# Optimization experiments

Measured on AMD Instinct MI355X. Metric: run time of the kernel, lower is better.

Reference implementation:

```python
import jax, jax.numpy as jnp
import numpy as np

IN_CH = 128
N_HEAD = 16
D_K = 4
D_MODEL = 256
T_PE = 1000.0
EPS = 1e-5


def setup_inputs() -> dict:
    key = jax.random.key(0)
    ks = jax.random.split(key, 8)
    sz_b, L, h, w = 4, 30, 64, 64
    x = jax.random.normal(ks[0], (sz_b, L, IN_CH, h, w), dtype=jnp.float32)
    batch_positions = jnp.sort(jax.random.randint(ks[1], (sz_b, L), 0, 365), axis=1).astype(jnp.int32)
    pad_mask = jnp.zeros((sz_b, L), dtype=bool)
    gn_weight = jnp.ones((IN_CH,), dtype=jnp.float32)
    gn_bias = jnp.zeros((IN_CH,), dtype=jnp.float32)
    conv_w = jax.random.normal(ks[2], (D_MODEL, IN_CH), dtype=jnp.float32) * (1.0 / np.sqrt(IN_CH))
    conv_b = jnp.zeros((D_MODEL,), dtype=jnp.float32)
    Q = jax.random.normal(ks[3], (N_HEAD, D_K), dtype=jnp.float32) * np.sqrt(2.0 / D_K)
    Wk = jax.random.normal(ks[4], (N_HEAD * D_K, D_MODEL), dtype=jnp.float32) * np.sqrt(2.0 / D_K)
    bk = jnp.zeros((N_HEAD * D_K,), dtype=jnp.float32)
    return {"x": x, "gn_weight": gn_weight, "gn_bias": gn_bias,
            "conv_w": conv_w, "conv_b": conv_b, "Q": Q, "Wk": Wk, "bk": bk,
            "batch_positions": batch_positions, "pad_mask": pad_mask}


def reference(x, gn_weight, gn_bias, conv_w, conv_b, Q, Wk, bk, batch_positions, pad_mask):
    n_head, d_k = Q.shape
    sz_b, L, d, h, w = x.shape
    B = sz_b * h * w
    # flatten pixels: [B, L, C]
    out = x.transpose(0, 3, 4, 1, 2).reshape(B, L, d)
    # GroupNorm(num_groups=n_head) over channels and time per pixel-sample
    g = out.transpose(0, 2, 1).reshape(B, n_head, d // n_head, L)
    mu = g.mean(axis=(2, 3), keepdims=True)
    var = g.var(axis=(2, 3), keepdims=True)
    g = (g - mu) / jnp.sqrt(var + EPS)
    out = g.reshape(B, d, L) * gn_weight[None, :, None] + gn_bias[None, :, None]
    out = out.transpose(0, 2, 1)  # [B, L, C]
    # 1x1 Conv1d == per-timestep linear projection to d_model
    out = out @ conv_w.T + conv_b  # [B, L, d_model]
    d_model = conv_w.shape[0]
    # sinusoidal positional encoding on dates, repeated over heads
    d_pe = d_model // n_head
    idx = jnp.arange(d_pe)
    denom = jnp.power(jnp.float32(T_PE), 2.0 * (idx // 2).astype(jnp.float32) / d_pe)
    tab = batch_positions.astype(jnp.float32)[:, :, None] / denom  # [sz_b, L, d_pe]
    pe = jnp.where(idx % 2 == 0, jnp.sin(tab), jnp.cos(tab))
    pe = jnp.tile(pe, (1, 1, n_head))  # [sz_b, L, d_model]
    out = (out.reshape(sz_b, h * w, L, d_model) + pe[:, None, :, :]).reshape(B, L, d_model)
    # keys and learned-query attention scores, temperature = sqrt(d_k)
    k = (out @ Wk.T + bk).reshape(B, L, n_head, d_k)
    scores = jnp.einsum('hd,blhd->hbl', Q, k) / jnp.sqrt(jnp.float32(d_k))
    scores = scores.reshape(n_head, sz_b, h * w, L)
    scores = jnp.where(pad_mask[None, :, None, :], jnp.float32(-1000.0), scores)
    attn = jax.nn.softmax(scores, axis=-1)
    # [n_head, sz_b, L, h, w]
    return attn.reshape(n_head, sz_b, h, w, L).transpose(0, 1, 4, 2, 3)
```

## Files before the change

kernel.cpp:

```cpp
#include <hip/hip_runtime.h>


#define EPSV 1e-5f

#define WS_U    0
#define WS_UU   2048
#define WS_P2   2304
#define WS_FLAG 4224
#define WS_QT   4352
#define WS_WT   8448
#define WS_INV  10496
#define WS_MUI  272640
#define PSF  1048576
#define PSQ  8912896

#define ACC4(S, Q, V) { (S).x += (V).x; (S).y += (V).y; (S).z += (V).z; (S).w += (V).w; \
                        (Q).x += (V).x*(V).x; (Q).y += (V).y*(V).y; (Q).z += (V).z*(V).z; (Q).w += (V).w*(V).w; }
#define FMA4(A, S, V) { (A).x += (S)*(V).x; (A).y += (S)*(V).y; (A).z += (S)*(V).z; (A).w += (S)*(V).w; }
#define NMA4(A, S, V) { (A).x -= (S)*(V).x; (A).y -= (S)*(V).y; (A).z -= (S)*(V).z; (A).w -= (S)*(V).w; }

__global__ void __launch_bounds__(256) k1a(const float* __restrict__ Q,
                                           const float* __restrict__ Wk,
                                           const float* __restrict__ conv_w,
                                           const float* __restrict__ gn_w,
                                           const float* __restrict__ conv_b,
                                           const float* __restrict__ gn_b,
                                           const float* __restrict__ bk,
                                           const int* __restrict__ bpos,
                                           const unsigned char* __restrict__ pmask,
                                           const float* __restrict__ x,
                                           float* __restrict__ ws) {
    int t = threadIdx.x;
    int bx = blockIdx.x;
    if (bx >= 480) {
        __shared__ float red[256];
        __shared__ float sc[16];
        __shared__ float qsv[256];
        __shared__ float rden[16];
        for (int i = t; i < 4096; i += 256) {
            int h = i >> 8, m = i & 255;
            float s = 0.f;
            #pragma unroll
            for (int d = 0; d < 4; ++d) s += Q[h*4+d] * Wk[(h*4+d)*256 + m];
            ws[WS_QT + h*256 + m] = s;
        }
        __syncthreads();
        for (int i = t; i < 2048; i += 256) {
            int h = i >> 7, c = i & 127;
            const float* qt = ws + WS_QT + h*256;
            float s = 0.f;
            #pragma unroll 32
            for (int m = 0; m < 256; ++m) s += qt[m] * conv_w[m*128 + c];
            ws[WS_WT + h*128 + c] = s;
            ws[WS_U  + c*16  + h] = s * gn_w[c];
        }
        __syncthreads();
        {
            int h = t >> 4, g2 = t & 15;
            float s = 0.f;
            #pragma unroll
            for (int cc = 0; cc < 8; ++cc) s += ws[WS_U + (g2*8+cc)*16 + h];
            ws[WS_UU + g2*16 + h] = s;
            float q = 0.f;
            #pragma unroll
            for (int r = 0; r < 16; ++r) q += ws[WS_QT + h*256 + r*16 + g2];
            qsv[h*16 + g2] = q;
        }
        {
            int h = t >> 4, p = t & 15;
            float s = 0.f;
            #pragma unroll
            for (int i = 0; i < 8; ++i) { int c = p*8+i; s += ws[WS_WT + h*128 + c] * gn_b[c]; }
            red[t] = s;
        }
        __syncthreads();
        if (t < 16) {
            float wb = 0.f;
            #pragma unroll
            for (int p = 0; p < 16; ++p) wb += red[t*16+p];
            sc[t] = wb;
        }
        __syncthreads();
        {
            int h = t >> 4, p = t & 15;
            float s = 0.f;
            #pragma unroll
            for (int i = 0; i < 16; ++i) { int m = p*16+i; s += ws[WS_QT + h*256 + m] * conv_b[m]; }
            red[t] = s;
        }
        __syncthreads();
        if (t < 16) {
            float s0 = 0.f;
            #pragma unroll
            for (int p = 0; p < 16; ++p) s0 += red[t*16+p];
            #pragma unroll
            for (int d = 0; d < 4; ++d) s0 += Q[t*4+d] * bk[t*4+d];
            sc[t] += s0;
            rden[t] = powf(1000.0f, -((float)(t >> 1)) * 0.125f);
        }
        if (t < 120) ws[WS_FLAG + t] = pmask[t] ? 1.f : 0.f;
        __syncthreads();
        for (int idx = t; idx < 1920; idx += 256) {
            int h = idx / 120, r = idx - h*120;
            float pos = (float)bpos[r];
            float pt = 0.f;
            #pragma unroll
            for (int p = 0; p < 16; ++p) {
                float tab = pos * rden[p];
                float v = (p & 1) ? cosf(tab) : sinf(tab);
                pt += v * qsv[h*16 + p];
            }
            ws[WS_P2 + r*16 + h] = pt + sc[h];
        }
        return;
    }
    int pb2 = bx / 30, l = bx - pb2*30;
    int pixbase = pb2 * 1024;
    int b = pixbase >> 12;
    int pijb = pixbase & 4095;
    int bl = b*30 + l;
    int pij = pijb + t*4;
    int pix0 = pixbase + t*4;
    const float* xbase = x + (bl*128)*4096 + pij;
    float* psb = ws + PSF + (l*16)*16384 + pix0;
    #pragma unroll 2
    for (int g = 0; g < 16; ++g) {
        const float* xg = xbase + g*8*4096;
        float4 s = make_float4(0.f,0.f,0.f,0.f);
        float4 q = make_float4(0.f,0.f,0.f,0.f);
        #pragma unroll
        for (int cc = 0; cc < 8; ++cc) {
            float4 v = *(const float4*)(xg + cc*4096);
            ACC4(s, q, v);
        }
        *(float4*)(psb + g*16384)              = s;
        *(float4*)(psb + g*16384 + (PSQ-PSF))  = q;
    }
}

__global__ void __launch_bounds__(256) k1r(float* __restrict__ ws) {
    int bx = blockIdx.x;
    int g = bx >> 4, pw = bx & 15;
    int pix = pw*1024 + threadIdx.x*4;
    const float* ps = ws + PSF + g*16384 + pix;
    float4 S = make_float4(0.f,0.f,0.f,0.f);
    float4 SS = make_float4(0.f,0.f,0.f,0.f);
    #pragma unroll 5
    for (int l = 0; l < 30; ++l) {
        float4 a = *(const float4*)(ps + l*16*16384);
        float4 b = *(const float4*)(ps + l*16*16384 + (PSQ-PSF));
        S.x += a.x; S.y += a.y; S.z += a.z; S.w += a.w;
        SS.x += b.x; SS.y += b.y; SS.z += b.z; SS.w += b.w;
    }
    float4 inv, mui;
    {
        float mu = S.x*(1.f/240.f); float va = SS.x*(1.f/240.f) - mu*mu;
        inv.x = rsqrtf(va + EPSV); mui.x = mu*inv.x;
        mu = S.y*(1.f/240.f); va = SS.y*(1.f/240.f) - mu*mu;
        inv.y = rsqrtf(va + EPSV); mui.y = mu*inv.y;
        mu = S.z*(1.f/240.f); va = SS.z*(1.f/240.f) - mu*mu;
        inv.z = rsqrtf(va + EPSV); mui.z = mu*inv.z;
        mu = S.w*(1.f/240.f); va = SS.w*(1.f/240.f) - mu*mu;
        inv.w = rsqrtf(va + EPSV); mui.w = mu*inv.w;
    }
    *(float4*)(ws + WS_INV + g*16384 + pix) = inv;
    *(float4*)(ws + WS_MUI + g*16384 + pix) = mui;
}

__global__ void __launch_bounds__(256) k2(const float* __restrict__ x,
                                          const float* __restrict__ ws,
                                          float* __restrict__ out) {
    __shared__ float su[2048];
    __shared__ float sU[256];
    __shared__ float sP2[16];
    __shared__ float sflag;
    int t = threadIdx.x;
    int bx = blockIdx.x;
    int pb2 = bx / 30, l = bx - pb2*30;
    int pixbase = pb2 * 1024;
    int b = pixbase >> 12;
    int pijb = pixbase & 4095;
    int bl = b*30 + l;
    int pij = pijb + t*4;
    int pix0 = pixbase + t*4;

    for (int i = t; i < 512; i += 256)
        *(float4*)(su + i*4) = *(const float4*)(ws + WS_U + i*4);
    sU[t] = ws[WS_UU + t];
    if (t < 16) sP2[t] = ws[WS_P2 + bl*16 + t];
    if (t == 0) sflag = ws[WS_FLAG + bl];
    __syncthreads();

    float4 acc[16];
    #pragma unroll
    for (int h = 0; h < 16; ++h) acc[h] = make_float4(0.f, 0.f, 0.f, 0.f);
    const float* xbase = x + (bl*128)*4096 + pij;
    #pragma unroll 2
    for (int g = 0; g < 16; ++g) {
        float4 inv = *(const float4*)(ws + WS_INV + g*16384 + pix0);
        float4 mui = *(const float4*)(ws + WS_MUI + g*16384 + pix0);
        const float* us = su + g*128;
        #pragma unroll
        for (int q = 0; q < 4; ++q) {
            float4 Ug = *(const float4*)(sU + g*16 + q*4);
            NMA4(acc[q*4+0], Ug.x, mui); NMA4(acc[q*4+1], Ug.y, mui);
            NMA4(acc[q*4+2], Ug.z, mui); NMA4(acc[q*4+3], Ug.w, mui);
        }
        const float* xg = xbase + g*8*4096;
        #pragma unroll
        for (int cc = 0; cc < 8; ++cc) {
            float4 v = *(const float4*)(xg + cc*4096);
            float4 xs;
            xs.x = v.x*inv.x; xs.y = v.y*inv.y; xs.z = v.z*inv.z; xs.w = v.w*inv.w;
            #pragma unroll
            for (int q = 0; q < 4; ++q) {
                float4 uq = *(const float4*)(us + cc*16 + q*4);
                FMA4(acc[q*4+0], uq.x, xs); FMA4(acc[q*4+1], uq.y, xs);
                FMA4(acc[q*4+2], uq.z, xs); FMA4(acc[q*4+3], uq.w, xs);
            }
        }
    }
    bool msk = (sflag != 0.f);
    #pragma unroll
    for (int h = 0; h < 16; ++h) {
        float p2 = sP2[h];
        float4 sv;
        sv.x = 0.5f*(acc[h].x + p2); sv.y = 0.5f*(acc[h].y + p2);
        sv.z = 0.5f*(acc[h].z + p2); sv.w = 0.5f*(acc[h].w + p2);
        if (msk) sv = make_float4(-1000.f, -1000.f, -1000.f, -1000.f);
        *(float4*)(out + ((h*4 + b)*30 + l)*4096 + pij) = sv;
    }
}

__global__ void __launch_bounds__(256) k3(float* __restrict__ out) {
    int idx = blockIdx.x*256 + threadIdx.x;
    int hb = idx >> 11;
    int pij = (idx & 2047)*2;
    float* p = out + hb*30*4096 + pij;
    float2 v[30];
    float m0 = -1e30f, m1 = -1e30f;
    #pragma unroll
    for (int l = 0; l < 30; ++l) {
        v[l] = *(const float2*)(p + l*4096);
        m0 = fmaxf(m0, v[l].x); m1 = fmaxf(m1, v[l].y);
    }
    float s0 = 0.f, s1 = 0.f;
    #pragma unroll
    for (int l = 0; l < 30; ++l) {
        v[l].x = __expf(v[l].x - m0); s0 += v[l].x;
        v[l].y = __expf(v[l].y - m1); s1 += v[l].y;
    }
    float r0 = 1.f/s0, r1 = 1.f/s1;
    #pragma unroll
    for (int l = 0; l < 30; ++l) {
        *(float2*)(p + l*4096) = make_float2(v[l].x*r0, v[l].y*r1);
    }
}

extern "C" void kernel_launch(void* const* d_in, const int* in_sizes, int n_in,
                              void* d_out, int out_size, void* d_ws, size_t ws_size,
                              hipStream_t stream) {
    const float* x      = (const float*)d_in[0];
    const float* gn_w   = (const float*)d_in[1];
    const float* gn_b   = (const float*)d_in[2];
    const float* conv_w = (const float*)d_in[3];
    const float* conv_b = (const float*)d_in[4];
    const float* Q      = (const float*)d_in[5];
    const float* Wk     = (const float*)d_in[6];
    const float* bk     = (const float*)d_in[7];
    const int*   bpos   = (const int*)d_in[8];
    const unsigned char* pmask = (const unsigned char*)d_in[9];
    float* ws  = (float*)d_ws;
    float* out = (float*)d_out;

    hipLaunchKernelGGL(k1a, dim3(481), dim3(256), 0, stream,
                       Q, Wk, conv_w, gn_w, conv_b, gn_b, bk, bpos, pmask, x, ws);
    hipLaunchKernelGGL(k1r, dim3(256), dim3(256), 0, stream, ws);
    hipLaunchKernelGGL(k2,  dim3(480), dim3(256), 0, stream, x, ws, out);
    hipLaunchKernelGGL(k3,  dim3(512), dim3(256), 0, stream, out);
}
```

Before: 171.5 us.

## Reduce GroupNorm partial sums over time first instead of channels

The first-pass statistics kernel now has each thread sum one channel over all 30 timesteps, producing per-channel partials, instead of summing the 8 channels of a group per timestep. The second pass then reduces 8 channel partials rather than 30 timestep partials, which shrinks the partial-sum workspace traffic. The grid grows from 480 to 2048 blocks for more parallelism. The trade-off is stride-heavy reads of x across timesteps.

```diff
diff --git a/kernel.cpp b/kernel.cpp
--- a/kernel.cpp
+++ b/kernel.cpp
@@ -12,14 +12,14 @@
 #define WS_INV  10496
 #define WS_MUI  272640
 #define PSF  1048576
-#define PSQ  8912896
-
-#define ACC4(S, Q, V) { (S).x += (V).x; (S).y += (V).y; (S).z += (V).z; (S).w += (V).w; \
-                        (Q).x += (V).x*(V).x; (Q).y += (V).y*(V).y; (Q).z += (V).z*(V).z; (Q).w += (V).w*(V).w; }
+#define PSQD 2097152
+
+#define ADD4(A, V)  { (A).x += (V).x; (A).y += (V).y; (A).z += (V).z; (A).w += (V).w; }
+#define ADDSQ4(A,V) { (A).x += (V).x*(V).x; (A).y += (V).y*(V).y; (A).z += (V).z*(V).z; (A).w += (V).w*(V).w; }
 #define FMA4(A, S, V) { (A).x += (S)*(V).x; (A).y += (S)*(V).y; (A).z += (S)*(V).z; (A).w += (S)*(V).w; }
 #define NMA4(A, S, V) { (A).x -= (S)*(V).x; (A).y -= (S)*(V).y; (A).z -= (S)*(V).z; (A).w -= (S)*(V).w; }
 
-__global__ void __launch_bounds__(256) k1a(const float* __restrict__ Q,
+__global__ void __launch_bounds__(256) k1s(const float* __restrict__ Q,
                                            const float* __restrict__ Wk,
                                            const float* __restrict__ conv_w,
                                            const float* __restrict__ gn_w,
@@ -32,7 +32,7 @@
                                            float* __restrict__ ws) {
     int t = threadIdx.x;
     int bx = blockIdx.x;
-    if (bx >= 480) {
+    if (bx >= 2048) {
         __shared__ float red[256];
         __shared__ float sc[16];
         __shared__ float qsv[256];
@@ -114,43 +114,37 @@
         }
         return;
     }
-    int pb2 = bx / 30, l = bx - pb2*30;
-    int pixbase = pb2 * 1024;
-    int b = pixbase >> 12;
-    int pijb = pixbase & 4095;
-    int bl = b*30 + l;
-    int pij = pijb + t*4;
-    int pix0 = pixbase + t*4;
-    const float* xbase = x + (bl*128)*4096 + pij;
-    float* psb = ws + PSF + (l*16)*16384 + pix0;
-    #pragma unroll 2
-    for (int g = 0; g < 16; ++g) {
-        const float* xg = xbase + g*8*4096;
-        float4 s = make_float4(0.f,0.f,0.f,0.f);
-        float4 q = make_float4(0.f,0.f,0.f,0.f);
-        #pragma unroll
-        for (int cc = 0; cc < 8; ++cc) {
-            float4 v = *(const float4*)(xg + cc*4096);
-            ACC4(s, q, v);
-        }
-        *(float4*)(psb + g*16384)              = s;
-        *(float4*)(psb + g*16384 + (PSQ-PSF))  = q;
-    }
+    int b = bx >> 9;
+    int rem = bx & 511;
+    int c = rem >> 2;
+    int w = rem & 3;
+    int pij = w*1024 + t*4;
+    const float* xp = x + ((b*30)*128 + c)*4096 + pij;
+    float4 s = make_float4(0.f,0.f,0.f,0.f);
+    float4 q = make_float4(0.f,0.f,0.f,0.f);
+    #pragma unroll
+    for (int l = 0; l < 30; ++l) {
+        float4 v = *(const float4*)(xp + l*524288);
+        ADD4(s, v); ADDSQ4(q, v);
+    }
+    float* ps = ws + PSF + (b*128 + c)*4096 + pij;
+    *(float4*)(ps)        = s;
+    *(float4*)(ps + PSQD) = q;
 }
 
 __global__ void __launch_bounds__(256) k1r(float* __restrict__ ws) {
     int bx = blockIdx.x;
-    int g = bx >> 4, pw = bx & 15;
-    int pix = pw*1024 + threadIdx.x*4;
-    const float* ps = ws + PSF + g*16384 + pix;
+    int g = bx >> 4, w = bx & 15;
+    int p0 = w*1024 + threadIdx.x*4;
+    int b = p0 >> 12, pij = p0 & 4095;
+    const float* base = ws + PSF + (b*128 + g*8)*4096 + pij;
     float4 S = make_float4(0.f,0.f,0.f,0.f);
     float4 SS = make_float4(0.f,0.f,0.f,0.f);
-    #pragma unroll 5
-    for (int l = 0; l < 30; ++l) {
-        float4 a = *(const float4*)(ps + l*16*16384);
-        float4 b = *(const float4*)(ps + l*16*16384 + (PSQ-PSF));
-        S.x += a.x; S.y += a.y; S.z += a.z; S.w += a.w;
-        SS.x += b.x; SS.y += b.y; SS.z += b.z; SS.w += b.w;
+    #pragma unroll
+    for (int cc = 0; cc < 8; ++cc) {
+        float4 a = *(const float4*)(base + cc*4096);
+        float4 bq = *(const float4*)(base + cc*4096 + PSQD);
+        ADD4(S, a); ADD4(SS, bq);
     }
     float4 inv, mui;
     {
@@ -163,8 +157,8 @@
         mu = S.w*(1.f/240.f); va = SS.w*(1.f/240.f) - mu*mu;
         inv.w = rsqrtf(va + EPSV); mui.w = mu*inv.w;
     }
-    *(float4*)(ws + WS_INV + g*16384 + pix) = inv;
-    *(float4*)(ws + WS_MUI + g*16384 + pix) = mui;
+    *(float4*)(ws + WS_INV + g*16384 + p0) = inv;
+    *(float4*)(ws + WS_MUI + g*16384 + p0) = mui;
 }
 
 __global__ void __launch_bounds__(256) k2(const float* __restrict__ x,
@@ -273,9 +267,9 @@
     float* ws  = (float*)d_ws;
     float* out = (float*)d_out;
 
-    hipLaunchKernelGGL(k1a, dim3(481), dim3(256), 0, stream,
+    hipLaunchKernelGGL(k1s, dim3(2049), dim3(256), 0, stream,
                        Q, Wk, conv_w, gn_w, conv_b, gn_b, bk, bpos, pmask, x, ws);
-    hipLaunchKernelGGL(k1r, dim3(256), dim3(256), 0, stream, ws);
-    hipLaunchKernelGGL(k2,  dim3(480), dim3(256), 0, stream, x, ws, out);
-    hipLaunchKernelGGL(k3,  dim3(512), dim3(256), 0, stream, out);
-}
+    hipLaunchKernelGGL(k1r, dim3(256),  dim3(256), 0, stream, ws);
+    hipLaunchKernelGGL(k2,  dim3(480),  dim3(256), 0, stream, x, ws, out);
+    hipLaunchKernelGGL(k3,  dim3(512),  dim3(256), 0, stream, out);
+}
```

Measured after the change: 171.3 us. About the same (-0.1%).
